# Performance work log

Hardware: AMD Instinct MI355X
Metric: run time of the kernel (lower is better)

Reference implementation:

```python
import jax, jax.numpy as jnp
import numpy as np

B, T, D, H = 2, 2048, 1024, 16
HD = D // H  # head dim = 64; rope half-dim = 32


def setup_inputs() -> dict:
    key = jax.random.key(0)
    ks = jax.random.split(key, 8)
    x = jax.random.normal(ks[0], (B, T, D), dtype=jnp.float32)
    # additive causal mask (upper triangle = -inf-like), as typically passed in
    mask = jnp.triu(jnp.full((T, T), -1e9, dtype=jnp.float32), k=1)
    # standard RoPE angles: theta = pos / 10000^(2i/hd)
    inv_freq = 1.0 / (10000.0 ** (np.arange(0, HD, 2, dtype=np.float32) / HD))
    ang = np.arange(T, dtype=np.float32)[:, None] * inv_freq[None, :]  # [T, HD//2]
    cos = jnp.asarray(np.cos(ang), dtype=jnp.float32)
    sin = jnp.asarray(np.sin(ang), dtype=jnp.float32)
    s = 1.0 / np.sqrt(D)
    Wq = jax.random.normal(ks[1], (D, D), dtype=jnp.float32) * s
    bq = jnp.zeros((D,), dtype=jnp.float32)
    Wk = jax.random.normal(ks[2], (D, D), dtype=jnp.float32) * s
    Wv = jax.random.normal(ks[3], (D, D), dtype=jnp.float32) * s
    bv = jnp.zeros((D,), dtype=jnp.float32)
    Wo = jax.random.normal(ks[4], (D, D), dtype=jnp.float32) * s
    bo = jnp.zeros((D,), dtype=jnp.float32)
    return {"x": x, "mask": mask, "cos": cos, "sin": sin, "Wq": Wq, "bq": bq,
            "Wk": Wk, "Wv": Wv, "bv": bv, "Wo": Wo, "bo": bo}


def _apply_rope(t, cos, sin):
    # t: [B, T, H, HD]; cos/sin: [T, HD//2]; complex multiply on (even, odd) pairs
    t = t.reshape(B, T, H, HD // 2, 2)
    t0, t1 = t[..., 0], t[..., 1]
    c = cos[None, :, None, :]
    s = sin[None, :, None, :]
    out = jnp.stack([t0 * c - t1 * s, t0 * s + t1 * c], axis=-1)
    return out.reshape(B, T, H, HD)


def reference(x, mask, cos, sin, Wq, bq, Wk, Wv, bv, Wo, bo):
    scale = float(HD) ** (-0.25)
    q = (x @ Wq.T + bq).reshape(B, T, H, HD)
    k = (x @ Wk.T).reshape(B, T, H, HD)  # key proj has no bias
    v = (x @ Wv.T + bv).reshape(B, T, H, HD)
    q = _apply_rope(q, cos, sin)
    k = _apply_rope(k, cos, sin)
    q = q.transpose(0, 2, 1, 3) * scale  # [B,H,T,HD]
    k = k.transpose(0, 2, 1, 3) * scale
    v = v.transpose(0, 2, 1, 3)
    qk = jnp.einsum("bhtd,bhsd->bhts", q, k) + mask  # [B,H,T,T]
    qk = qk.astype(jnp.float32)
    w = jax.nn.softmax(qk, axis=-1).astype(q.dtype)
    wv = jnp.einsum("bhts,bhsd->bhtd", w, v)
    wv = wv.transpose(0, 2, 1, 3).reshape(B, T, D)
    out = wv @ Wo.T + bo
    return out, qk
```

## Files before the change

kernel.cpp:

```cpp
#include <hip/hip_runtime.h>
#include <math.h>

#define Tc 2048
#define Dc 1024
#define Hc 16
#define HDc 64
#define BT 4096
#define SCALE 0.35355339059327379f

typedef _Float16 f16;
typedef __attribute__((ext_vector_type(4))) _Float16 f16x4;
typedef __attribute__((ext_vector_type(8))) _Float16 f16x8;
typedef __attribute__((ext_vector_type(4))) float f32x4;

__global__ __launch_bounds__(256)
void cast1_kernel(const float* __restrict__ in, f16* __restrict__ out, int n4)
{
    int i = blockIdx.x * 256 + threadIdx.x;
    if (i < n4) {
        float4 v = ((const float4*)in)[i];
        f16x4 o = {(f16)v.x, (f16)v.y, (f16)v.z, (f16)v.w};
        ((f16x4*)out)[i] = o;
    }
}

__global__ __launch_bounds__(256)
void cast4_kernel(const float* __restrict__ s0, const float* __restrict__ s1,
                  const float* __restrict__ s2, const float* __restrict__ s3,
                  f16* __restrict__ d0, f16* __restrict__ d1,
                  f16* __restrict__ d2, f16* __restrict__ d3, int n4)
{
    const float* s; f16* d;
    switch (blockIdx.y) {
        case 0:  s = s0; d = d0; break;
        case 1:  s = s1; d = d1; break;
        case 2:  s = s2; d = d2; break;
        default: s = s3; d = d3; break;
    }
    int i = blockIdx.x * 256 + threadIdx.x;
    if (i < n4) {
        float4 v = ((const float4*)s)[i];
        f16x4 o = {(f16)v.x, (f16)v.y, (f16)v.z, (f16)v.w};
        ((f16x4*)d)[i] = o;
    }
}

__global__ __launch_bounds__(256)
void qkv_proj_kernel(const f16* __restrict__ xh,
                     const f16* __restrict__ Wqh, const f16* __restrict__ Wkh,
                     const f16* __restrict__ Wvh,
                     const float* __restrict__ bq, const float* __restrict__ bv,
                     f16* __restrict__ qh, f16* __restrict__ kh, f16* __restrict__ vh,
                     const float* __restrict__ cosp, const float* __restrict__ sinp)
{
    const int mode = blockIdx.z;
    const f16* W = (mode == 0) ? Wqh : (mode == 1 ? Wkh : Wvh);
    const float* bias = (mode == 0) ? bq : (mode == 2 ? bv : nullptr);
    f16* dst = (mode == 0) ? qh : (mode == 1 ? kh : vh);

    __shared__ f16 As[128][40];
    __shared__ f16 Ws[64][40];
    const int tid = threadIdx.x;
    const int w = tid >> 6, l = tid & 63;
    const int lr = l & 15, lq = l >> 4;
    const int m0 = blockIdx.y * 128, n0 = blockIdx.x * 64;

    f32x4 acc[2][4] = {};

    for (int k0 = 0; k0 < Dc; k0 += 32) {
        __syncthreads();
        {
            int r = tid >> 1, c = (tid & 1) * 16;
            *(f16x8*)&As[r][c]     = *(const f16x8*)&xh[(size_t)(m0 + r) * Dc + k0 + c];
            *(f16x8*)&As[r][c + 8] = *(const f16x8*)&xh[(size_t)(m0 + r) * Dc + k0 + c + 8];
            int rw = tid >> 2, cw = (tid & 3) * 8;
            *(f16x8*)&Ws[rw][cw] = *(const f16x8*)&W[(size_t)(n0 + rw) * Dc + k0 + cw];
        }
        __syncthreads();
        f16x8 af[2], bf[4];
        #pragma unroll
        for (int mi = 0; mi < 2; mi++) af[mi] = *(const f16x8*)&As[32 * w + 16 * mi + lr][lq * 8];
        #pragma unroll
        for (int ni = 0; ni < 4; ni++) bf[ni] = *(const f16x8*)&Ws[16 * ni + lr][lq * 8];
        #pragma unroll
        for (int mi = 0; mi < 2; mi++)
            #pragma unroll
            for (int ni = 0; ni < 4; ni++)
                acc[mi][ni] = __builtin_amdgcn_mfma_f32_16x16x32_f16(af[mi], bf[ni], acc[mi][ni], 0, 0, 0);
    }

    #pragma unroll
    for (int mi = 0; mi < 2; mi++) {
        #pragma unroll
        for (int ni = 0; ni < 4; ni++) {
            #pragma unroll
            for (int i = 0; i < 4; i++) {
                int gm = m0 + 32 * w + 16 * mi + lq * 4 + i;
                int gn = n0 + 16 * ni + lr;
                float v = acc[mi][ni][i];
                if (bias) v += bias[gn];
                int b = gm >> 11, t = gm & 2047;
                int h = gn >> 6, d = gn & 63;
                if (mode != 2) {
                    float pv = __shfl_xor(v, 1, 64);
                    int p = d >> 1;
                    float c = cosp[t * 32 + p], s = sinp[t * 32 + p];
                    v = (d & 1) ? (pv * s + v * c) : (v * c - pv * s);
                    v *= SCALE;
                }
                dst[((size_t)(b * Hc + h) * Tc + t) * HDc + d] = (f16)v;
            }
        }
    }
}

__global__ __launch_bounds__(256)
void out_proj_kernel(const f16* __restrict__ A, const f16* __restrict__ W,
                     const float* __restrict__ bias, float* __restrict__ out)
{
    __shared__ f16 As[128][40];
    __shared__ f16 Ws[64][40];
    const int tid = threadIdx.x;
    const int w = tid >> 6, l = tid & 63;
    const int lr = l & 15, lq = l >> 4;
    const int m0 = blockIdx.y * 128, n0 = blockIdx.x * 64;

    f32x4 acc[2][4] = {};

    for (int k0 = 0; k0 < Dc; k0 += 32) {
        __syncthreads();
        {
            int r = tid >> 1, c = (tid & 1) * 16;
            *(f16x8*)&As[r][c]     = *(const f16x8*)&A[(size_t)(m0 + r) * Dc + k0 + c];
            *(f16x8*)&As[r][c + 8] = *(const f16x8*)&A[(size_t)(m0 + r) * Dc + k0 + c + 8];
            int rw = tid >> 2, cw = (tid & 3) * 8;
            *(f16x8*)&Ws[rw][cw] = *(const f16x8*)&W[(size_t)(n0 + rw) * Dc + k0 + cw];
        }
        __syncthreads();
        f16x8 af[2], bf[4];
        #pragma unroll
        for (int mi = 0; mi < 2; mi++) af[mi] = *(const f16x8*)&As[32 * w + 16 * mi + lr][lq * 8];
        #pragma unroll
        for (int ni = 0; ni < 4; ni++) bf[ni] = *(const f16x8*)&Ws[16 * ni + lr][lq * 8];
        #pragma unroll
        for (int mi = 0; mi < 2; mi++)
            #pragma unroll
            for (int ni = 0; ni < 4; ni++)
                acc[mi][ni] = __builtin_amdgcn_mfma_f32_16x16x32_f16(af[mi], bf[ni], acc[mi][ni], 0, 0, 0);
    }

    #pragma unroll
    for (int mi = 0; mi < 2; mi++)
        #pragma unroll
        for (int ni = 0; ni < 4; ni++)
            #pragma unroll
            for (int i = 0; i < 4; i++) {
                int gm = m0 + 32 * w + 16 * mi + lq * 4 + i;
                int gn = n0 + 16 * ni + lr;
                out[(size_t)gm * Dc + gn] = acc[mi][ni][i] + bias[gn];
            }
}

__global__ __launch_bounds__(256)
void qk_kernel(const f16* __restrict__ qh, const f16* __restrict__ kh,
               float* __restrict__ qk)
{
    const int z = blockIdx.z;
    const int t0 = blockIdx.y * 128, s0 = blockIdx.x * 64;
    float* C = qk + (size_t)z * Tc * Tc;
    const int tid = threadIdx.x;

    if (s0 > t0 + 127) {
        int r = tid >> 1, cb = (tid & 1) * 32;
        float4 mv; mv.x = mv.y = mv.z = mv.w = -1e9f;
        float4* row = (float4*)(C + (size_t)(t0 + r) * Tc + s0 + cb);
        #pragma unroll
        for (int j = 0; j < 8; j++) row[j] = mv;
        return;
    }

    __shared__ f16 Qs[128][72];
    __shared__ f16 Ks[64][72];
    const int w = tid >> 6, l = tid & 63;
    const int lr = l & 15, lq = l >> 4;
    const f16* Qg = qh + (size_t)z * Tc * HDc;
    const f16* Kg = kh + (size_t)z * Tc * HDc;
    {
        int r = tid >> 1, c = (tid & 1) * 32;
        #pragma unroll
        for (int j = 0; j < 4; j++)
            *(f16x8*)&Qs[r][c + 8 * j] = *(const f16x8*)&Qg[(size_t)(t0 + r) * HDc + c + 8 * j];
        int rk = tid >> 2, ck = (tid & 3) * 16;
        *(f16x8*)&Ks[rk][ck]     = *(const f16x8*)&Kg[(size_t)(s0 + rk) * HDc + ck];
        *(f16x8*)&Ks[rk][ck + 8] = *(const f16x8*)&Kg[(size_t)(s0 + rk) * HDc + ck + 8];
    }
    __syncthreads();

    f32x4 acc[2][4] = {};
    #pragma unroll
    for (int ks = 0; ks < 2; ks++) {
        f16x8 af[2], bf[4];
        #pragma unroll
        for (int mi = 0; mi < 2; mi++) af[mi] = *(const f16x8*)&Qs[32 * w + 16 * mi + lr][lq * 8 + 32 * ks];
        #pragma unroll
        for (int ni = 0; ni < 4; ni++) bf[ni] = *(const f16x8*)&Ks[16 * ni + lr][lq * 8 + 32 * ks];
        #pragma unroll
        for (int mi = 0; mi < 2; mi++)
            #pragma unroll
            for (int ni = 0; ni < 4; ni++)
                acc[mi][ni] = __builtin_amdgcn_mfma_f32_16x16x32_f16(af[mi], bf[ni], acc[mi][ni], 0, 0, 0);
    }

    #pragma unroll
    for (int mi = 0; mi < 2; mi++)
        #pragma unroll
        for (int ni = 0; ni < 4; ni++)
            #pragma unroll
            for (int i = 0; i < 4; i++) {
                int t = t0 + 32 * w + 16 * mi + lq * 4 + i;
                int s = s0 + 16 * ni + lr;
                float v = acc[mi][ni][i];
                if (s > t) v -= 1e9f;
                C[(size_t)t * Tc + s] = v;
            }
}

__global__ __launch_bounds__(256)
void flash_kernel(const f16* __restrict__ qh, const f16* __restrict__ kh,
                  const f16* __restrict__ vh, f16* __restrict__ wvh)
{
    const int z = blockIdx.y;
    const int t0 = (gridDim.x - 1 - blockIdx.x) * 64;
    const int tid = threadIdx.x;
    const int w = tid >> 6, l = tid & 63;
    const int lr = l & 15, lq = l >> 4;

    __shared__ f16 Qs[64][72];
    __shared__ f16 Ks[64][72];
    __shared__ f16 VsT[64][72];
    __shared__ f16 Ps[64][72];

    const f16* Qg = qh + (size_t)z * Tc * HDc;
    const f16* Kg = kh + (size_t)z * Tc * HDc;
    const f16* Vg = vh + (size_t)z * Tc * HDc;

    {
        int r = tid >> 2, c = (tid & 3) * 16;
        *(f16x8*)&Qs[r][c]     = *(const f16x8*)&Qg[(size_t)(t0 + r) * HDc + c];
        *(f16x8*)&Qs[r][c + 8] = *(const f16x8*)&Qg[(size_t)(t0 + r) * HDc + c + 8];
    }

    f32x4 O[4] = {};
    float mrow[4], lrow[4];
    #pragma unroll
    for (int i = 0; i < 4; i++) { mrow[i] = -1e30f; lrow[i] = 0.f; }

    for (int s0 = 0; s0 <= t0; s0 += 64) {
        __syncthreads();
        {
            int r = tid >> 2, c = (tid & 3) * 16;
            *(f16x8*)&Ks[r][c]     = *(const f16x8*)&Kg[(size_t)(s0 + r) * HDc + c];
            *(f16x8*)&Ks[r][c + 8] = *(const f16x8*)&Kg[(size_t)(s0 + r) * HDc + c + 8];
        }
        {
            int s = tid & 63, d0 = (tid >> 6) * 16;
            const f16* vp = &Vg[(size_t)(s0 + s) * HDc + d0];
            f16x8 v0 = *(const f16x8*)vp;
            f16x8 v1 = *(const f16x8*)(vp + 8);
            #pragma unroll
            for (int j = 0; j < 8; j++) {
                VsT[d0 + j][s]     = v0[j];
                VsT[d0 + 8 + j][s] = v1[j];
            }
        }
        __syncthreads();

        f32x4 S[4] = {};
        #pragma unroll
        for (int ks = 0; ks < 2; ks++) {
            f16x8 aq = *(const f16x8*)&Qs[16 * w + lr][lq * 8 + 32 * ks];
            #pragma unroll
            for (int ni = 0; ni < 4; ni++) {
                f16x8 bk = *(const f16x8*)&Ks[16 * ni + lr][lq * 8 + 32 * ks];
                S[ni] = __builtin_amdgcn_mfma_f32_16x16x32_f16(aq, bk, S[ni], 0, 0, 0);
            }
        }

        if (s0 == t0) {
            #pragma unroll
            for (int ni = 0; ni < 4; ni++)
                #pragma unroll
                for (int i = 0; i < 4; i++) {
                    int tg = t0 + 16 * w + lq * 4 + i;
                    int sg = s0 + 16 * ni + lr;
                    if (sg > tg) S[ni][i] = -1e9f;
                }
        }

        #pragma unroll
        for (int i = 0; i < 4; i++) {
            float v = fmaxf(fmaxf(S[0][i], S[1][i]), fmaxf(S[2][i], S[3][i]));
            v = fmaxf(v, __shfl_xor(v, 1, 64));
            v = fmaxf(v, __shfl_xor(v, 2, 64));
            v = fmaxf(v, __shfl_xor(v, 4, 64));
            v = fmaxf(v, __shfl_xor(v, 8, 64));
            float mnew = fmaxf(mrow[i], v);
            float alpha = __expf(mrow[i] - mnew);
            mrow[i] = mnew;
            float rs = 0.f;
            #pragma unroll
            for (int ni = 0; ni < 4; ni++) {
                float p = __expf(S[ni][i] - mnew);
                S[ni][i] = p;
                rs += p;
            }
            rs += __shfl_xor(rs, 1, 64);
            rs += __shfl_xor(rs, 2, 64);
            rs += __shfl_xor(rs, 4, 64);
            rs += __shfl_xor(rs, 8, 64);
            lrow[i] = lrow[i] * alpha + rs;
            #pragma unroll
            for (int ni = 0; ni < 4; ni++) O[ni][i] *= alpha;
        }

        #pragma unroll
        for (int ni = 0; ni < 4; ni++)
            #pragma unroll
            for (int i = 0; i < 4; i++)
                Ps[16 * w + lq * 4 + i][16 * ni + lr] = (f16)S[ni][i];

        #pragma unroll
        for (int ks = 0; ks < 2; ks++) {
            f16x8 ap = *(const f16x8*)&Ps[16 * w + lr][lq * 8 + 32 * ks];
            #pragma unroll
            for (int ni = 0; ni < 4; ni++) {
                f16x8 bv = *(const f16x8*)&VsT[16 * ni + lr][lq * 8 + 32 * ks];
                O[ni] = __builtin_amdgcn_mfma_f32_16x16x32_f16(ap, bv, O[ni], 0, 0, 0);
            }
        }
    }

    const int b = z >> 4, h = z & 15;
    #pragma unroll
    for (int ni = 0; ni < 4; ni++)
        #pragma unroll
        for (int i = 0; i < 4; i++) {
            int tg = t0 + 16 * w + lq * 4 + i;
            int d = 16 * ni + lr;
            float o = O[ni][i] / lrow[i];
            wvh[((size_t)(b * Tc + tg)) * Dc + h * HDc + d] = (f16)o;
        }
}

extern "C" void kernel_launch(void* const* d_in, const int* in_sizes, int n_in,
                              void* d_out, int out_size, void* d_ws, size_t ws_size,
                              hipStream_t stream)
{
    const float* x    = (const float*)d_in[0];
    const float* cosp = (const float*)d_in[2];
    const float* sinp = (const float*)d_in[3];
    const float* Wq   = (const float*)d_in[4];
    const float* bq   = (const float*)d_in[5];
    const float* Wk   = (const float*)d_in[6];
    const float* Wv   = (const float*)d_in[7];
    const float* bv   = (const float*)d_in[8];
    const float* Wo   = (const float*)d_in[9];
    const float* bo   = (const float*)d_in[10];

    float* out = (float*)d_out;
    float* qk  = out + (size_t)BT * Dc;

    f16* ws  = (f16*)d_ws;
    f16* xh  = ws;
    f16* Wqh = xh  + (size_t)BT * Dc;
    f16* Wkh = Wqh + (size_t)Dc * Dc;
    f16* Wvh = Wkh + (size_t)Dc * Dc;
    f16* Woh = Wvh + (size_t)Dc * Dc;
    f16* qh  = Woh + (size_t)Dc * Dc;
    f16* kh  = qh  + (size_t)BT * Dc;
    f16* vh  = kh  + (size_t)BT * Dc;
    f16* wvh = vh  + (size_t)BT * Dc;

    dim3 blk(256);

    cast1_kernel<<<dim3(BT * Dc / 1024), blk, 0, stream>>>(x, xh, BT * Dc / 4);
    cast4_kernel<<<dim3(Dc * Dc / 1024, 4), blk, 0, stream>>>(
        Wq, Wk, Wv, Wo, Wqh, Wkh, Wvh, Woh, Dc * Dc / 4);

    qkv_proj_kernel<<<dim3(Dc / 64, BT / 128, 3), blk, 0, stream>>>(
        xh, Wqh, Wkh, Wvh, bq, bv, qh, kh, vh, cosp, sinp);

    qk_kernel<<<dim3(Tc / 64, Tc / 128, 32), blk, 0, stream>>>(qh, kh, qk);

    flash_kernel<<<dim3(Tc / 64, 32), blk, 0, stream>>>(qh, kh, vh, wvh);

    out_proj_kernel<<<dim3(Dc / 64, BT / 128), blk, 0, stream>>>(wvh, Woh, bo, out);
}
```

Baseline: 859.5 us.

## Fuse QK logits output into flash attention kernel and drop separate qk kernel

Removes the standalone qk_kernel and has the flash attention kernel write the masked QK scores to the qk output as it computes them. Each block also fills the fully masked part of its rows with -1e9. This avoids recomputing Q·K^T and reloading Q/K in a second launch. In exchange, the large qk write now comes from fewer, causally unbalanced flash blocks, and its strided scalar stores sit inside the softmax loop.

```diff
diff --git a/kernel.cpp b/kernel.cpp
--- a/kernel.cpp
+++ b/kernel.cpp
@@ -162,72 +162,9 @@
 }
 
 __global__ __launch_bounds__(256)
-void qk_kernel(const f16* __restrict__ qh, const f16* __restrict__ kh,
-               float* __restrict__ qk)
-{
-    const int z = blockIdx.z;
-    const int t0 = blockIdx.y * 128, s0 = blockIdx.x * 64;
-    float* C = qk + (size_t)z * Tc * Tc;
-    const int tid = threadIdx.x;
-
-    if (s0 > t0 + 127) {
-        int r = tid >> 1, cb = (tid & 1) * 32;
-        float4 mv; mv.x = mv.y = mv.z = mv.w = -1e9f;
-        float4* row = (float4*)(C + (size_t)(t0 + r) * Tc + s0 + cb);
-        #pragma unroll
-        for (int j = 0; j < 8; j++) row[j] = mv;
-        return;
-    }
-
-    __shared__ f16 Qs[128][72];
-    __shared__ f16 Ks[64][72];
-    const int w = tid >> 6, l = tid & 63;
-    const int lr = l & 15, lq = l >> 4;
-    const f16* Qg = qh + (size_t)z * Tc * HDc;
-    const f16* Kg = kh + (size_t)z * Tc * HDc;
-    {
-        int r = tid >> 1, c = (tid & 1) * 32;
-        #pragma unroll
-        for (int j = 0; j < 4; j++)
-            *(f16x8*)&Qs[r][c + 8 * j] = *(const f16x8*)&Qg[(size_t)(t0 + r) * HDc + c + 8 * j];
-        int rk = tid >> 2, ck = (tid & 3) * 16;
-        *(f16x8*)&Ks[rk][ck]     = *(const f16x8*)&Kg[(size_t)(s0 + rk) * HDc + ck];
-        *(f16x8*)&Ks[rk][ck + 8] = *(const f16x8*)&Kg[(size_t)(s0 + rk) * HDc + ck + 8];
-    }
-    __syncthreads();
-
-    f32x4 acc[2][4] = {};
-    #pragma unroll
-    for (int ks = 0; ks < 2; ks++) {
-        f16x8 af[2], bf[4];
-        #pragma unroll
-        for (int mi = 0; mi < 2; mi++) af[mi] = *(const f16x8*)&Qs[32 * w + 16 * mi + lr][lq * 8 + 32 * ks];
-        #pragma unroll
-        for (int ni = 0; ni < 4; ni++) bf[ni] = *(const f16x8*)&Ks[16 * ni + lr][lq * 8 + 32 * ks];
-        #pragma unroll
-        for (int mi = 0; mi < 2; mi++)
-            #pragma unroll
-            for (int ni = 0; ni < 4; ni++)
-                acc[mi][ni] = __builtin_amdgcn_mfma_f32_16x16x32_f16(af[mi], bf[ni], acc[mi][ni], 0, 0, 0);
-    }
-
-    #pragma unroll
-    for (int mi = 0; mi < 2; mi++)
-        #pragma unroll
-        for (int ni = 0; ni < 4; ni++)
-            #pragma unroll
-            for (int i = 0; i < 4; i++) {
-                int t = t0 + 32 * w + 16 * mi + lq * 4 + i;
-                int s = s0 + 16 * ni + lr;
-                float v = acc[mi][ni][i];
-                if (s > t) v -= 1e9f;
-                C[(size_t)t * Tc + s] = v;
-            }
-}
-
-__global__ __launch_bounds__(256)
 void flash_kernel(const f16* __restrict__ qh, const f16* __restrict__ kh,
-                  const f16* __restrict__ vh, f16* __restrict__ wvh)
+                  const f16* __restrict__ vh, f16* __restrict__ wvh,
+                  float* __restrict__ qk)
 {
     const int z = blockIdx.y;
     const int t0 = (gridDim.x - 1 - blockIdx.x) * 64;
@@ -243,11 +180,20 @@
     const f16* Qg = qh + (size_t)z * Tc * HDc;
     const f16* Kg = kh + (size_t)z * Tc * HDc;
     const f16* Vg = vh + (size_t)z * Tc * HDc;
+    float* C = qk + (size_t)z * Tc * Tc;
 
     {
         int r = tid >> 2, c = (tid & 3) * 16;
         *(f16x8*)&Qs[r][c]     = *(const f16x8*)&Qg[(size_t)(t0 + r) * HDc + c];
         *(f16x8*)&Qs[r][c + 8] = *(const f16x8*)&Qg[(size_t)(t0 + r) * HDc + c + 8];
+    }
+
+    {
+        int r = t0 + (tid >> 2);
+        int n4 = (Tc - t0 - 64) >> 2;
+        float4 mv; mv.x = mv.y = mv.z = mv.w = -1e9f;
+        float4* rowp = (float4*)(C + (size_t)r * Tc + t0 + 64);
+        for (int c = (tid & 3); c < n4; c += 4) rowp[c] = mv;
     }
 
     f32x4 O[4] = {};
@@ -296,6 +242,15 @@
                     if (sg > tg) S[ni][i] = -1e9f;
                 }
         }
+
+        #pragma unroll
+        for (int ni = 0; ni < 4; ni++)
+            #pragma unroll
+            for (int i = 0; i < 4; i++) {
+                int tg = t0 + 16 * w + lq * 4 + i;
+                int sg = s0 + 16 * ni + lr;
+                C[(size_t)tg * Tc + sg] = S[ni][i];
+            }
 
         #pragma unroll
         for (int i = 0; i < 4; i++) {
@@ -390,9 +345,7 @@
     qkv_proj_kernel<<<dim3(Dc / 64, BT / 128, 3), blk, 0, stream>>>(
         xh, Wqh, Wkh, Wvh, bq, bv, qh, kh, vh, cosp, sinp);
 
-    qk_kernel<<<dim3(Tc / 64, Tc / 128, 32), blk, 0, stream>>>(qh, kh, qk);
-
-    flash_kernel<<<dim3(Tc / 64, 32), blk, 0, stream>>>(qh, kh, vh, wvh);
+    flash_kernel<<<dim3(Tc / 64, 32), blk, 0, stream>>>(qh, kh, vh, wvh, qk);
 
     out_proj_kernel<<<dim3(Dc / 64, BT / 128), blk, 0, stream>>>(wvh, Woh, bo, out);
 }
```

Result: faster. 779.6 us (-9.3%).
